# Optimization experiments

Measured on AMD Instinct MI355X. Metric: run time of the kernel, lower is better.

Reference implementation:

```python
import jax, jax.numpy as jnp
import numpy as np

N_USER = 50000
N_ITEM = 50000
D_IN = 128
D_OUT = 128
N_EDGE = 600000


def _sage(x_src, x_dst, ei, Wl, bl, Wr):
    # PyG SAGEConv: out = lin_l(mean_{j in N(i)} x_j) + lin_r(x_i)
    # lin_l has bias, lin_r has no bias. Weights are [out, in].
    src, dst = ei[0], ei[1]
    n_dst = x_dst.shape[0]
    msg = x_src[src]                                            # [E, D_in] gather
    agg = jax.ops.segment_sum(msg, dst, num_segments=n_dst)     # [N_dst, D_in]
    cnt = jax.ops.segment_sum(jnp.ones((ei.shape[1],), x_src.dtype), dst,
                              num_segments=n_dst)
    mean = agg / jnp.maximum(cnt, 1.0)[:, None]                 # isolated nodes -> 0
    return mean @ Wl.T + bl + x_dst @ Wr.T


def setup_inputs() -> dict:
    key = jax.random.key(0)
    ks = jax.random.split(key, 16)
    inp = {
        "x_user": jax.random.normal(ks[0], (N_USER, D_IN), jnp.float32),
        "x_item": jax.random.normal(ks[1], (N_ITEM, D_IN), jnp.float32),
        "ei_rates": jax.random.randint(ks[2], (2, N_EDGE), 0, N_USER, jnp.int64 if jax.config.jax_enable_x64 else jnp.int32),
        "ei_rev": jax.random.randint(ks[3], (2, N_EDGE), 0, N_USER, jnp.int64 if jax.config.jax_enable_x64 else jnp.int32),
        "ei_follows": jax.random.randint(ks[4], (2, N_EDGE), 0, N_USER, jnp.int64 if jax.config.jax_enable_x64 else jnp.int32),
    }
    s = 1.0 / np.sqrt(D_IN)
    names = ["rates", "rev", "fol"]
    for i, nm in enumerate(names):
        inp[f"Wl_{nm}"] = jax.random.uniform(ks[5 + 3 * i], (D_OUT, D_IN), jnp.float32, -s, s)
        inp[f"bl_{nm}"] = jax.random.uniform(ks[6 + 3 * i], (D_OUT,), jnp.float32, -s, s)
        inp[f"Wr_{nm}"] = jax.random.uniform(ks[7 + 3 * i], (D_OUT, D_IN), jnp.float32, -s, s)
    return inp


def reference(x_user, x_item, ei_rates, ei_rev, ei_follows,
              Wl_rates, bl_rates, Wr_rates,
              Wl_rev, bl_rev, Wr_rev,
              Wl_fol, bl_fol, Wr_fol):
    # relation (user -rates-> item): src=user, dst=item
    out_item = _sage(x_user, x_item, ei_rates, Wl_rates, bl_rates, Wr_rates)
    # relation (item -rev_rates-> user): src=item, dst=user
    out_user_rev = _sage(x_item, x_user, ei_rev, Wl_rev, bl_rev, Wr_rev)
    # relation (user -follows-> user)
    out_user_fol = _sage(x_user, x_user, ei_follows, Wl_fol, bl_fol, Wr_fol)
    # HeteroConv aggr='mean': average relation outputs per dst node type
    out_user = (out_user_rev + out_user_fol) * 0.5
    return out_user, out_item
```

## Files before the change

kernel.cpp:

```cpp
#include <hip/hip_runtime.h>

#define D 128
#define NBB 392

typedef __attribute__((ext_vector_type(8))) short bf16x8;
typedef __attribute__((ext_vector_type(4))) float f32x4;

__device__ inline unsigned short f2bf(float f) {
  unsigned u = __builtin_bit_cast(unsigned, f);
  unsigned r = u + 0x7FFFu + ((u >> 16) & 1u);
  return (unsigned short)(r >> 16);
}
__device__ inline float bf2f(unsigned short b) {
  unsigned u = ((unsigned)b) << 16;
  return __builtin_bit_cast(float, u);
}

struct SetupArgs {
  const float* xu; const float* xi;
  unsigned short* xbu; unsigned short* xbi;
  int n4u, n4i, nbConv;
  const int* ei[3]; int ne[3]; int nbh[3]; int nbHist;
  int* bh;
  const float* Wl_rates; const float* Wr_rates; const float* bl_rates;
  const float* Wl_rev;   const float* Wr_rev;   const float* bl_rev;
  const float* Wl_fol;   const float* Wr_fol;   const float* bl_fol;
  unsigned short* Wb_user; unsigned short* Wb_item;
  float* b_user; float* b_item;
};

__global__ void __launch_bounds__(256) setup_kernel(SetupArgs S) {
  const int tid = threadIdx.x;
  int b = blockIdx.x;
  if (b < S.nbConv) {
    int i = b * 256 + tid;
    const float* x;
    unsigned short* xb;
    if (i < S.n4u) { x = S.xu; xb = S.xbu; }
    else { i -= S.n4u; if (i >= S.n4i) return; x = S.xi; xb = S.xbi; }
    float4 v = ((const float4*)x)[i];
    ushort4 o;
    o.x = f2bf(v.x); o.y = f2bf(v.y); o.z = f2bf(v.z); o.w = f2bf(v.w);
    ((ushort4*)xb)[i] = o;
    return;
  }
  b -= S.nbConv;
  if (b < S.nbHist) {
    int rel = 0;
    while (b >= S.nbh[rel]) { b -= S.nbh[rel]; rel++; }
    __shared__ int lh[NBB];
    for (int t = tid; t < NBB; t += 256) lh[t] = 0;
    __syncthreads();
    const int ne = S.ne[rel];
    const int* dsts = S.ei[rel] + ne;
    const int base = b * 2048;
#pragma unroll
    for (int k = 0; k < 8; k++) {
      int i = base + k * 256 + tid;
      if (i < ne) atomicAdd(&lh[dsts[i] >> 7], 1);
    }
    __syncthreads();
    for (int t = tid; t < NBB; t += 256)
      if (lh[t]) atomicAdd(&S.bh[rel * NBB + t], lh[t]);
    return;
  }
  b -= S.nbHist;
  int idx = b * 256 + tid;
  if (idx >= 128 * 384) return;
  int n = idx / 384, k = idx - n * 384;
  float v;
  if (k < 128)      v = 0.5f * S.Wl_rev[n * 128 + k];
  else if (k < 256) v = 0.5f * S.Wl_fol[n * 128 + (k - 128)];
  else              v = 0.5f * (S.Wr_rev[n * 128 + (k - 256)] + S.Wr_fol[n * 128 + (k - 256)]);
  S.Wb_user[n * 384 + k] = f2bf(v);
  if (k < 256) {
    float w = (k < 128) ? S.Wl_rates[n * 128 + k] : S.Wr_rates[n * 128 + (k - 128)];
    S.Wb_item[n * 256 + k] = f2bf(w);
  }
  if (idx < 128) {
    S.b_item[idx] = S.bl_rates[idx];
    S.b_user[idx] = 0.5f * (S.bl_rev[idx] + S.bl_fol[idx]);
  }
}

__global__ void __launch_bounds__(192) scanb_kernel(const int* __restrict__ bh,
                                                    int* __restrict__ bbase,
                                                    int* __restrict__ bcur, int nbkt) {
  int w = threadIdx.x >> 6, l = threadIdx.x & 63;
  if (w >= 3) return;
  const int off = w * NBB;
  int v[7];
  int s0 = 0;
#pragma unroll
  for (int k = 0; k < 7; k++) {
    int idx = l * 7 + k;
    v[k] = (idx < nbkt) ? bh[off + idx] : 0;
    s0 += v[k];
  }
  int s = s0;
  for (int dlt = 1; dlt < 64; dlt <<= 1) {
    int t = __shfl_up(s, dlt);
    if (l >= dlt) s += t;
  }
  int run = s - s0;
#pragma unroll
  for (int k = 0; k < 7; k++) {
    int idx = l * 7 + k;
    if (idx < nbkt) { bbase[off + idx] = run; bcur[off + idx] = run; run += v[k]; }
  }
  if (l == 63) bbase[off + nbkt] = run;
}

struct PArgs { const int* ei[3]; int ne[3]; int nb[3]; unsigned* part[3]; };

__global__ void __launch_bounds__(256) part_kernel(PArgs P, int* __restrict__ bcur,
                                                   int nbkt) {
  int b = blockIdx.x, rel = 0;
  while (b >= P.nb[rel]) { b -= P.nb[rel]; rel++; }
  const int ne = P.ne[rel];
  const int* src = P.ei[rel];
  const int* dst = src + ne;
  const int base = b * 4096;
  const int tn = min(4096, ne - base);
  __shared__ int lh[NBB], lscan[NBB], gb[NBB], lcur[NBB];
  __shared__ uint2 pairs[4096];
  const int tid = threadIdx.x;
  for (int t = tid; t < NBB; t += 256) lh[t] = 0;
  __syncthreads();
#pragma unroll
  for (int k = 0; k < 16; k++) {
    int i = base + k * 256 + tid;
    if (i < ne) atomicAdd(&lh[dst[i] >> 7], 1);
  }
  __syncthreads();
  if (tid < 64) {
    int v[7];
    int s0 = 0;
#pragma unroll
    for (int k = 0; k < 7; k++) {
      int idx = tid * 7 + k;
      v[k] = (idx < NBB) ? lh[idx] : 0;
      s0 += v[k];
    }
    int s = s0;
    for (int dlt = 1; dlt < 64; dlt <<= 1) {
      int t = __shfl_up(s, dlt);
      if (tid >= dlt) s += t;
    }
    int run = s - s0;
#pragma unroll
    for (int k = 0; k < 7; k++) {
      int idx = tid * 7 + k;
      if (idx < NBB) { lscan[idx] = run; run += v[k]; }
    }
  }
  __syncthreads();
  for (int t = tid; t < nbkt; t += 256) {
    int c = lh[t];
    gb[t] = c ? atomicAdd(&bcur[rel * NBB + t], c) : 0;
    lcur[t] = lscan[t];
  }
  __syncthreads();
#pragma unroll
  for (int k = 0; k < 16; k++) {
    int i = base + k * 256 + tid;
    if (i < ne) {
      int d = dst[i];
      int slot = atomicAdd(&lcur[d >> 7], 1);
      pairs[slot] = (uint2){(unsigned)src[i], (unsigned)d};
    }
  }
  __syncthreads();
  unsigned* __restrict__ out = P.part[rel];
#pragma unroll
  for (int k = 0; k < 16; k++) {
    int slot = k * 256 + tid;
    if (slot < tn) {
      uint2 p = pairs[slot];
      int bin = (int)(p.y >> 7);
      out[gb[bin] + (slot - lscan[bin])] = p.x | ((p.y & 127u) << 25);
    }
  }
}

struct BAArgs {
  const unsigned* part[3];
  const unsigned short* xb[3];
  unsigned short* mean[3];
  int m[3];
};

__global__ void __launch_bounds__(512) bagg_kernel(BAArgs A, const int* __restrict__ bbase,
                                                   int nbkt) {
  const int rel = blockIdx.x / nbkt;
  const int b = blockIdx.x - rel * nbkt;
  const int bs = bbase[rel * NBB + b];
  const int be = bbase[rel * NBB + b + 1];
  const int n = be - bs;
  const unsigned* __restrict__ pp = A.part[rel] + bs;
  const unsigned short* __restrict__ x = A.xb[rel];
  unsigned short* __restrict__ mean = A.mean[rel];
  const int m = A.m[rel];
  const int tid = threadIdx.x;
  const int w = tid >> 6, lane = tid & 63;
  const size_t loff = (size_t)lane * 2;
  __shared__ unsigned sorted[4096];
  __shared__ int lcnt[128], lofs[128], lcur[128];

  if (n > 4096) {
    for (int r = w; r < 128; r += 8) {
      int gdst = b * 128 + r;
      if (gdst >= m) break;
      float a0 = 0.f, a1 = 0.f;
      int cnt = 0;
      for (int j = 0; j < n; j++) {
        unsigned p = pp[j];
        if ((int)(p >> 25) == r) {
          unsigned v = *(const unsigned*)(x + (size_t)(p & 0x1FFFFFFu) * D + loff);
          a0 += bf2f((unsigned short)(v & 0xFFFFu));
          a1 += bf2f((unsigned short)(v >> 16));
          cnt++;
        }
      }
      float inv = 1.0f / (float)max(cnt, 1);
      unsigned o = (unsigned)f2bf(a0 * inv) | ((unsigned)f2bf(a1 * inv) << 16);
      *(unsigned*)(mean + (size_t)gdst * D + loff) = o;
    }
    return;
  }

  if (tid < 128) lcnt[tid] = 0;
  __syncthreads();
  for (int i = tid; i < n; i += 512) atomicAdd(&lcnt[pp[i] >> 25], 1);
  __syncthreads();
  if (tid < 64) {
    int v0 = lcnt[2 * tid], v1 = lcnt[2 * tid + 1];
    int s0 = v0 + v1, s = s0;
    for (int dlt = 1; dlt < 64; dlt <<= 1) {
      int t = __shfl_up(s, dlt);
      if (tid >= dlt) s += t;
    }
    int ex = s - s0;
    lofs[2 * tid] = ex;
    lofs[2 * tid + 1] = ex + v0;
  }
  __syncthreads();
  if (tid < 128) lcur[tid] = lofs[tid];
  __syncthreads();
  for (int i = tid; i < n; i += 512) {
    unsigned p = pp[i];
    int slot = atomicAdd(&lcur[p >> 25], 1);
    sorted[slot] = p;
  }
  __syncthreads();

  const int r0 = w * 16, r1 = r0 + 16;
  int j = lofs[r0];
  const int jend = lcur[r1 - 1];
  int cur = r0;
  float a0 = 0.f, a1 = 0.f;

  auto putrow = [&](int r, float s0, float s1) {
    int g = b * 128 + r;
    if (g < m) {
      float inv = 1.0f / (float)max(lcur[r] - lofs[r], 1);
      unsigned o = (unsigned)f2bf(s0 * inv) | ((unsigned)f2bf(s1 * inv) << 16);
      *(unsigned*)(mean + (size_t)g * D + loff) = o;
    }
  };

#define STEP(pk, vk)                                                     \
  {                                                                      \
    int rk = (int)((pk) >> 25);                                          \
    if (rk != cur) {                                                     \
      putrow(cur, a0, a1);                                               \
      for (int z = cur + 1; z < rk; z++) putrow(z, 0.f, 0.f);            \
      cur = rk; a0 = 0.f; a1 = 0.f;                                      \
    }                                                                    \
    a0 += bf2f((unsigned short)((vk) & 0xFFFFu));                        \
    a1 += bf2f((unsigned short)((vk) >> 16));                            \
  }

  while (j + 8 <= jend) {
    unsigned p0 = sorted[j],     p1 = sorted[j + 1];
    unsigned p2 = sorted[j + 2], p3 = sorted[j + 3];
    unsigned p4 = sorted[j + 4], p5 = sorted[j + 5];
    unsigned p6 = sorted[j + 6], p7 = sorted[j + 7];
    unsigned v0 = *(const unsigned*)(x + (size_t)(p0 & 0x1FFFFFFu) * D + loff);
    unsigned v1 = *(const unsigned*)(x + (size_t)(p1 & 0x1FFFFFFu) * D + loff);
    unsigned v2 = *(const unsigned*)(x + (size_t)(p2 & 0x1FFFFFFu) * D + loff);
    unsigned v3 = *(const unsigned*)(x + (size_t)(p3 & 0x1FFFFFFu) * D + loff);
    unsigned v4 = *(const unsigned*)(x + (size_t)(p4 & 0x1FFFFFFu) * D + loff);
    unsigned v5 = *(const unsigned*)(x + (size_t)(p5 & 0x1FFFFFFu) * D + loff);
    unsigned v6 = *(const unsigned*)(x + (size_t)(p6 & 0x1FFFFFFu) * D + loff);
    unsigned v7 = *(const unsigned*)(x + (size_t)(p7 & 0x1FFFFFFu) * D + loff);
    STEP(p0, v0) STEP(p1, v1) STEP(p2, v2) STEP(p3, v3)
    STEP(p4, v4) STEP(p5, v5) STEP(p6, v6) STEP(p7, v7)
    j += 8;
  }
  for (; j < jend; j++) {
    unsigned p = sorted[j];
    unsigned v = *(const unsigned*)(x + (size_t)(p & 0x1FFFFFFu) * D + loff);
    STEP(p, v)
  }
#undef STEP
  putrow(cur, a0, a1);
  for (int z = cur + 1; z < r1; z++) putrow(z, 0.f, 0.f);
}

struct BSrcs { const unsigned short* s[3]; };
struct GemmArgs {
  BSrcs su, si;
  const unsigned short* wbU; const unsigned short* wbI;
  const float* bU; const float* bI;
  float* outU; float* outI;
  int MU, MI, nbU;
};

__global__ void __launch_bounds__(256) gemm2_kernel(GemmArgs A) {
  const bool isU = (int)blockIdx.x < A.nbU;
  const int bid = isU ? blockIdx.x : blockIdx.x - A.nbU;
  const BSrcs S = isU ? A.su : A.si;
  const unsigned short* __restrict__ Wb = isU ? A.wbU : A.wbI;
  const int K = isU ? 384 : 256;
  const float* __restrict__ bias = isU ? A.bU : A.bI;
  float* __restrict__ out = isU ? A.outU : A.outI;
  const int M = isU ? A.MU : A.MI;

  __shared__ __align__(16) unsigned short As[128][72];
  __shared__ __align__(16) unsigned short Ws[128][72];
  const int tid = threadIdx.x;
  const int lane = tid & 63;
  const int wave = tid >> 6;
  const int wr = (wave >> 1) * 64;
  const int wc = (wave & 1) * 64;
  const int l15 = lane & 15;
  const int quad = lane >> 4;
  const int m0 = bid * 128;

  f32x4 acc[4][4];
#pragma unroll
  for (int r = 0; r < 4; r++)
#pragma unroll
    for (int c = 0; c < 4; c++) acc[r][c] = (f32x4){0.f, 0.f, 0.f, 0.f};

  const int srow = tid >> 1, shalf = tid & 1;
  const int nchunks = K >> 6;
  for (int ch = 0; ch < nchunks; ch++) {
    const unsigned short* sp = S.s[ch >> 1];
    const int coff = (ch & 1) << 6;
    {
      int mm = min(m0 + srow, M - 1);
      const uint4* g = (const uint4*)(sp + (size_t)mm * D + coff + shalf * 32);
      uint4* ld = (uint4*)(&As[srow][shalf * 32]);
      ld[0] = g[0]; ld[1] = g[1]; ld[2] = g[2]; ld[3] = g[3];
    }
    {
      const uint4* g = (const uint4*)(Wb + (size_t)srow * K + ch * 64 + shalf * 32);
      uint4* ld = (uint4*)(&Ws[srow][shalf * 32]);
      ld[0] = g[0]; ld[1] = g[1]; ld[2] = g[2]; ld[3] = g[3];
    }
    __syncthreads();
#pragma unroll
    for (int kk = 0; kk < 64; kk += 32) {
      const int kb = kk + quad * 8;
      bf16x8 a0 = *(const bf16x8*)&As[wr + l15][kb];
      bf16x8 a1 = *(const bf16x8*)&As[wr + 16 + l15][kb];
      bf16x8 a2 = *(const bf16x8*)&As[wr + 32 + l15][kb];
      bf16x8 a3 = *(const bf16x8*)&As[wr + 48 + l15][kb];
      bf16x8 b0 = *(const bf16x8*)&Ws[wc + l15][kb];
      bf16x8 b1 = *(const bf16x8*)&Ws[wc + 16 + l15][kb];
      bf16x8 b2 = *(const bf16x8*)&Ws[wc + 32 + l15][kb];
      bf16x8 b3 = *(const bf16x8*)&Ws[wc + 48 + l15][kb];
      acc[0][0] = __builtin_amdgcn_mfma_f32_16x16x32_bf16(a0, b0, acc[0][0], 0, 0, 0);
      acc[0][1] = __builtin_amdgcn_mfma_f32_16x16x32_bf16(a0, b1, acc[0][1], 0, 0, 0);
      acc[0][2] = __builtin_amdgcn_mfma_f32_16x16x32_bf16(a0, b2, acc[0][2], 0, 0, 0);
      acc[0][3] = __builtin_amdgcn_mfma_f32_16x16x32_bf16(a0, b3, acc[0][3], 0, 0, 0);
      acc[1][0] = __builtin_amdgcn_mfma_f32_16x16x32_bf16(a1, b0, acc[1][0], 0, 0, 0);
      acc[1][1] = __builtin_amdgcn_mfma_f32_16x16x32_bf16(a1, b1, acc[1][1], 0, 0, 0);
      acc[1][2] = __builtin_amdgcn_mfma_f32_16x16x32_bf16(a1, b2, acc[1][2], 0, 0, 0);
      acc[1][3] = __builtin_amdgcn_mfma_f32_16x16x32_bf16(a1, b3, acc[1][3], 0, 0, 0);
      acc[2][0] = __builtin_amdgcn_mfma_f32_16x16x32_bf16(a2, b0, acc[2][0], 0, 0, 0);
      acc[2][1] = __builtin_amdgcn_mfma_f32_16x16x32_bf16(a2, b1, acc[2][1], 0, 0, 0);
      acc[2][2] = __builtin_amdgcn_mfma_f32_16x16x32_bf16(a2, b2, acc[2][2], 0, 0, 0);
      acc[2][3] = __builtin_amdgcn_mfma_f32_16x16x32_bf16(a2, b3, acc[2][3], 0, 0, 0);
      acc[3][0] = __builtin_amdgcn_mfma_f32_16x16x32_bf16(a3, b0, acc[3][0], 0, 0, 0);
      acc[3][1] = __builtin_amdgcn_mfma_f32_16x16x32_bf16(a3, b1, acc[3][1], 0, 0, 0);
      acc[3][2] = __builtin_amdgcn_mfma_f32_16x16x32_bf16(a3, b2, acc[3][2], 0, 0, 0);
      acc[3][3] = __builtin_amdgcn_mfma_f32_16x16x32_bf16(a3, b3, acc[3][3], 0, 0, 0);
    }
    __syncthreads();
  }
#pragma unroll
  for (int c = 0; c < 4; c++) {
    const int n = wc + c * 16 + l15;
    const float bv = bias[n];
#pragma unroll
    for (int r = 0; r < 4; r++) {
      const int mrow = m0 + wr + r * 16 + quad * 4;
#pragma unroll
      for (int i = 0; i < 4; i++) {
        if (mrow + i < M) out[(size_t)(mrow + i) * D + n] = acc[r][c][i] + bv;
      }
    }
  }
}

extern "C" void kernel_launch(void* const* d_in, const int* in_sizes, int n_in,
                              void* d_out, int out_size, void* d_ws, size_t ws_size,
                              hipStream_t stream) {
  const float* x_user   = (const float*)d_in[0];
  const float* x_item   = (const float*)d_in[1];
  const int*   ei_rates = (const int*)d_in[2];
  const int*   ei_rev   = (const int*)d_in[3];
  const int*   ei_fol   = (const int*)d_in[4];
  const float* Wl_rates = (const float*)d_in[5];
  const float* bl_rates = (const float*)d_in[6];
  const float* Wr_rates = (const float*)d_in[7];
  const float* Wl_rev   = (const float*)d_in[8];
  const float* bl_rev   = (const float*)d_in[9];
  const float* Wr_rev   = (const float*)d_in[10];
  const float* Wl_fol   = (const float*)d_in[11];
  const float* bl_fol   = (const float*)d_in[12];
  const float* Wr_fol   = (const float*)d_in[13];

  const int NU = in_sizes[0] / D;
  const int NI = in_sizes[1] / D;
  const int E_rates = in_sizes[2] / 2;
  const int E_rev   = in_sizes[3] / 2;
  const int E_fol   = in_sizes[4] / 2;
  const int nbkt = ((NU > NI ? NU : NI) + 127) / 128;

  char* wsb = (char*)d_ws;
  size_t off = 0;
  auto take = [&](size_t bytes) {
    char* p = wsb + off;
    off += (bytes + 15) & ~(size_t)15;
    return p;
  };
  int* bhist = (int*)take(3 * NBB * 4);
  const size_t zero_bytes = off;
  int* bbase = (int*)take(3 * NBB * 4);
  int* bcur  = (int*)take(3 * NBB * 4);
  unsigned* part_rates = (unsigned*)take((size_t)E_rates * 4);
  unsigned* part_rev   = (unsigned*)take((size_t)E_rev * 4);
  unsigned* part_fol   = (unsigned*)take((size_t)E_fol * 4);
  unsigned short* xb_user    = (unsigned short*)take((size_t)NU * D * 2);
  unsigned short* xb_item    = (unsigned short*)take((size_t)NI * D * 2);
  unsigned short* mean_rates = (unsigned short*)take((size_t)NI * D * 2);
  unsigned short* mean_rev   = (unsigned short*)take((size_t)NU * D * 2);
  unsigned short* mean_fol   = (unsigned short*)take((size_t)NU * D * 2);
  unsigned short* Wb_user    = (unsigned short*)take(128 * 384 * 2);
  unsigned short* Wb_item    = (unsigned short*)take(128 * 256 * 2);
  float* b_user = (float*)take(128 * 4);
  float* b_item = (float*)take(128 * 4);

  hipMemsetAsync(d_ws, 0, zero_bytes, stream);

  SetupArgs SA;
  SA.xu = x_user; SA.xi = x_item; SA.xbu = xb_user; SA.xbi = xb_item;
  SA.n4u = NU * D / 4; SA.n4i = NI * D / 4;
  SA.nbConv = (SA.n4u + SA.n4i + 255) / 256;
  SA.ei[0] = ei_rates; SA.ne[0] = E_rates; SA.nbh[0] = (E_rates + 2047) / 2048;
  SA.ei[1] = ei_rev;   SA.ne[1] = E_rev;   SA.nbh[1] = (E_rev + 2047) / 2048;
  SA.ei[2] = ei_fol;   SA.ne[2] = E_fol;   SA.nbh[2] = (E_fol + 2047) / 2048;
  SA.nbHist = SA.nbh[0] + SA.nbh[1] + SA.nbh[2];
  SA.bh = bhist;
  SA.Wl_rates = Wl_rates; SA.Wr_rates = Wr_rates; SA.bl_rates = bl_rates;
  SA.Wl_rev = Wl_rev; SA.Wr_rev = Wr_rev; SA.bl_rev = bl_rev;
  SA.Wl_fol = Wl_fol; SA.Wr_fol = Wr_fol; SA.bl_fol = bl_fol;
  SA.Wb_user = Wb_user; SA.Wb_item = Wb_item;
  SA.b_user = b_user; SA.b_item = b_item;
  const int nbPrep = (128 * 384 + 255) / 256;
  setup_kernel<<<SA.nbConv + SA.nbHist + nbPrep, 256, 0, stream>>>(SA);

  scanb_kernel<<<1, 192, 0, stream>>>(bhist, bbase, bcur, nbkt);

  PArgs P;
  P.ei[0] = ei_rates; P.ne[0] = E_rates; P.nb[0] = (E_rates + 4095) / 4096; P.part[0] = part_rates;
  P.ei[1] = ei_rev;   P.ne[1] = E_rev;   P.nb[1] = (E_rev + 4095) / 4096;   P.part[1] = part_rev;
  P.ei[2] = ei_fol;   P.ne[2] = E_fol;   P.nb[2] = (E_fol + 4095) / 4096;   P.part[2] = part_fol;
  part_kernel<<<P.nb[0] + P.nb[1] + P.nb[2], 256, 0, stream>>>(P, bcur, nbkt);

  BAArgs BA;
  BA.part[0] = part_rates; BA.xb[0] = xb_user; BA.mean[0] = mean_rates; BA.m[0] = NI;
  BA.part[1] = part_rev;   BA.xb[1] = xb_item; BA.mean[1] = mean_rev;   BA.m[1] = NU;
  BA.part[2] = part_fol;   BA.xb[2] = xb_user; BA.mean[2] = mean_fol;   BA.m[2] = NU;
  bagg_kernel<<<3 * nbkt, 512, 0, stream>>>(BA, bbase, nbkt);

  GemmArgs gma;
  gma.su.s[0] = mean_rev;   gma.su.s[1] = mean_fol; gma.su.s[2] = xb_user;
  gma.si.s[0] = mean_rates; gma.si.s[1] = xb_item;  gma.si.s[2] = nullptr;
  gma.wbU = Wb_user; gma.wbI = Wb_item;
  gma.bU = b_user;   gma.bI = b_item;
  gma.outU = (float*)d_out;
  gma.outI = (float*)d_out + (size_t)NU * D;
  gma.MU = NU; gma.MI = NI;
  gma.nbU = (NU + 127) / 128;
  const int nbI = (NI + 127) / 128;
  gemm2_kernel<<<gma.nbU + nbI, 256, 0, stream>>>(gma);
}
```

Measured before the change: 314.1 us.

## Split bucket aggregation into separate sort and fine-grained gather kernels

The fused bucket-aggregate kernel is replaced by two kernels. A sort kernel orders each bucket's edges by destination row into global memory and records CSR row starts. A gather kernel then uses many smaller blocks, each covering 64 rows, to do the mean aggregation. This drops the 16KB shared-memory buffer and the slow fallback path for buckets over 4096 edges, and raises occupancy and the number of blocks for the gather. The cost is an extra launch and a global round-trip of the sorted edge arrays.

```diff
diff --git a/kernel.cpp b/kernel.cpp
--- a/kernel.cpp
+++ b/kernel.cpp
@@ -183,55 +183,29 @@
   }
 }
 
-struct BAArgs {
+struct SortArgs {
   const unsigned* part[3];
-  const unsigned short* xb[3];
-  unsigned short* mean[3];
-  int m[3];
+  unsigned* sg[3];
+  int* rowstart;
+  int Rp1;
 };
 
-__global__ void __launch_bounds__(512) bagg_kernel(BAArgs A, const int* __restrict__ bbase,
+__global__ void __launch_bounds__(256) sort_kernel(SortArgs S, const int* __restrict__ bbase,
                                                    int nbkt) {
   const int rel = blockIdx.x / nbkt;
   const int b = blockIdx.x - rel * nbkt;
   const int bs = bbase[rel * NBB + b];
   const int be = bbase[rel * NBB + b + 1];
   const int n = be - bs;
-  const unsigned* __restrict__ pp = A.part[rel] + bs;
-  const unsigned short* __restrict__ x = A.xb[rel];
-  unsigned short* __restrict__ mean = A.mean[rel];
-  const int m = A.m[rel];
+  const unsigned* __restrict__ pp = S.part[rel] + bs;
+  unsigned* __restrict__ out = S.sg[rel] + bs;
+  int* __restrict__ rs = S.rowstart + rel * S.Rp1;
   const int tid = threadIdx.x;
-  const int w = tid >> 6, lane = tid & 63;
-  const size_t loff = (size_t)lane * 2;
-  __shared__ unsigned sorted[4096];
   __shared__ int lcnt[128], lofs[128], lcur[128];
 
-  if (n > 4096) {
-    for (int r = w; r < 128; r += 8) {
-      int gdst = b * 128 + r;
-      if (gdst >= m) break;
-      float a0 = 0.f, a1 = 0.f;
-      int cnt = 0;
-      for (int j = 0; j < n; j++) {
-        unsigned p = pp[j];
-        if ((int)(p >> 25) == r) {
-          unsigned v = *(const unsigned*)(x + (size_t)(p & 0x1FFFFFFu) * D + loff);
-          a0 += bf2f((unsigned short)(v & 0xFFFFu));
-          a1 += bf2f((unsigned short)(v >> 16));
-          cnt++;
-        }
-      }
-      float inv = 1.0f / (float)max(cnt, 1);
-      unsigned o = (unsigned)f2bf(a0 * inv) | ((unsigned)f2bf(a1 * inv) << 16);
-      *(unsigned*)(mean + (size_t)gdst * D + loff) = o;
-    }
-    return;
-  }
-
   if (tid < 128) lcnt[tid] = 0;
   __syncthreads();
-  for (int i = tid; i < n; i += 512) atomicAdd(&lcnt[pp[i] >> 25], 1);
+  for (int i = tid; i < n; i += 256) atomicAdd(&lcnt[pp[i] >> 25], 1);
   __syncthreads();
   if (tid < 64) {
     int v0 = lcnt[2 * tid], v1 = lcnt[2 * tid + 1];
@@ -245,25 +219,51 @@
     lofs[2 * tid + 1] = ex + v0;
   }
   __syncthreads();
-  if (tid < 128) lcur[tid] = lofs[tid];
-  __syncthreads();
-  for (int i = tid; i < n; i += 512) {
+  if (tid < 128) {
+    lcur[tid] = lofs[tid];
+    rs[b * 128 + tid] = bs + lofs[tid];
+  }
+  if (tid == 128 && b == nbkt - 1) rs[nbkt * 128] = be;
+  __syncthreads();
+  for (int i = tid; i < n; i += 256) {
     unsigned p = pp[i];
     int slot = atomicAdd(&lcur[p >> 25], 1);
-    sorted[slot] = p;
-  }
-  __syncthreads();
-
-  const int r0 = w * 16, r1 = r0 + 16;
-  int j = lofs[r0];
-  const int jend = lcur[r1 - 1];
-  int cur = r0;
+    out[slot] = p;
+  }
+}
+
+struct GArgs {
+  const unsigned* sg[3];
+  const unsigned short* xb[3];
+  unsigned short* mean[3];
+  int m[3];
+};
+
+__global__ void __launch_bounds__(256) gather_kernel(GArgs A, const int* __restrict__ rowstart,
+                                                     int nbpr, int Rp1) {
+  const int rel = blockIdx.x / nbpr;
+  const int blk = blockIdx.x - rel * nbpr;
+  const unsigned* __restrict__ sg = A.sg[rel];
+  const unsigned short* __restrict__ x = A.xb[rel];
+  unsigned short* __restrict__ mean = A.mean[rel];
+  const int m = A.m[rel];
+  const int* __restrict__ rs = rowstart + rel * Rp1;
+  const int tid = threadIdx.x;
+  const int w = tid >> 6, lane = tid & 63;
+  const size_t loff = (size_t)lane * 2;
+
+  const int gbase = blk * 64 + w * 16;
+  const int f0 = gbase & 127;
+  const int bkt = gbase - f0;
+  int j = rs[gbase];
+  const int jend = rs[gbase + 16];
+  int cur = f0;
   float a0 = 0.f, a1 = 0.f;
 
-  auto putrow = [&](int r, float s0, float s1) {
-    int g = b * 128 + r;
+  auto putrow = [&](int rf, float s0, float s1) {
+    int g = bkt + rf;
     if (g < m) {
-      float inv = 1.0f / (float)max(lcur[r] - lofs[r], 1);
+      float inv = 1.0f / (float)max(rs[g + 1] - rs[g], 1);
       unsigned o = (unsigned)f2bf(s0 * inv) | ((unsigned)f2bf(s1 * inv) << 16);
       *(unsigned*)(mean + (size_t)g * D + loff) = o;
     }
@@ -282,10 +282,10 @@
   }
 
   while (j + 8 <= jend) {
-    unsigned p0 = sorted[j],     p1 = sorted[j + 1];
-    unsigned p2 = sorted[j + 2], p3 = sorted[j + 3];
-    unsigned p4 = sorted[j + 4], p5 = sorted[j + 5];
-    unsigned p6 = sorted[j + 6], p7 = sorted[j + 7];
+    unsigned p0 = sg[j],     p1 = sg[j + 1];
+    unsigned p2 = sg[j + 2], p3 = sg[j + 3];
+    unsigned p4 = sg[j + 4], p5 = sg[j + 5];
+    unsigned p6 = sg[j + 6], p7 = sg[j + 7];
     unsigned v0 = *(const unsigned*)(x + (size_t)(p0 & 0x1FFFFFFu) * D + loff);
     unsigned v1 = *(const unsigned*)(x + (size_t)(p1 & 0x1FFFFFFu) * D + loff);
     unsigned v2 = *(const unsigned*)(x + (size_t)(p2 & 0x1FFFFFFu) * D + loff);
@@ -299,13 +299,13 @@
     j += 8;
   }
   for (; j < jend; j++) {
-    unsigned p = sorted[j];
+    unsigned p = sg[j];
     unsigned v = *(const unsigned*)(x + (size_t)(p & 0x1FFFFFFu) * D + loff);
     STEP(p, v)
   }
 #undef STEP
   putrow(cur, a0, a1);
-  for (int z = cur + 1; z < r1; z++) putrow(z, 0.f, 0.f);
+  for (int z = cur + 1; z < f0 + 16; z++) putrow(z, 0.f, 0.f);
 }
 
 struct BSrcs { const unsigned short* s[3]; };
@@ -430,6 +430,9 @@
   const int E_rev   = in_sizes[3] / 2;
   const int E_fol   = in_sizes[4] / 2;
   const int nbkt = ((NU > NI ? NU : NI) + 127) / 128;
+  const int Rtot = nbkt * 128;
+  const int Rp1 = Rtot + 1;
+  const int nbpr = Rtot / 64;
 
   char* wsb = (char*)d_ws;
   size_t off = 0;
@@ -445,6 +448,10 @@
   unsigned* part_rates = (unsigned*)take((size_t)E_rates * 4);
   unsigned* part_rev   = (unsigned*)take((size_t)E_rev * 4);
   unsigned* part_fol   = (unsigned*)take((size_t)E_fol * 4);
+  unsigned* sg_rates   = (unsigned*)take((size_t)E_rates * 4);
+  unsigned* sg_rev     = (unsigned*)take((size_t)E_rev * 4);
+  unsigned* sg_fol     = (unsigned*)take((size_t)E_fol * 4);
+  int* rowstart        = (int*)take((size_t)3 * Rp1 * 4);
   unsigned short* xb_user    = (unsigned short*)take((size_t)NU * D * 2);
   unsigned short* xb_item    = (unsigned short*)take((size_t)NI * D * 2);
   unsigned short* mean_rates = (unsigned short*)take((size_t)NI * D * 2);
@@ -482,11 +489,18 @@
   P.ei[2] = ei_fol;   P.ne[2] = E_fol;   P.nb[2] = (E_fol + 4095) / 4096;   P.part[2] = part_fol;
   part_kernel<<<P.nb[0] + P.nb[1] + P.nb[2], 256, 0, stream>>>(P, bcur, nbkt);
 
-  BAArgs BA;
-  BA.part[0] = part_rates; BA.xb[0] = xb_user; BA.mean[0] = mean_rates; BA.m[0] = NI;
-  BA.part[1] = part_rev;   BA.xb[1] = xb_item; BA.mean[1] = mean_rev;   BA.m[1] = NU;
-  BA.part[2] = part_fol;   BA.xb[2] = xb_user; BA.mean[2] = mean_fol;   BA.m[2] = NU;
-  bagg_kernel<<<3 * nbkt, 512, 0, stream>>>(BA, bbase, nbkt);
+  SortArgs SS;
+  SS.part[0] = part_rates; SS.sg[0] = sg_rates;
+  SS.part[1] = part_rev;   SS.sg[1] = sg_rev;
+  SS.part[2] = part_fol;   SS.sg[2] = sg_fol;
+  SS.rowstart = rowstart; SS.Rp1 = Rp1;
+  sort_kernel<<<3 * nbkt, 256, 0, stream>>>(SS, bbase, nbkt);
+
+  GArgs GA;
+  GA.sg[0] = sg_rates; GA.xb[0] = xb_user; GA.mean[0] = mean_rates; GA.m[0] = NI;
+  GA.sg[1] = sg_rev;   GA.xb[1] = xb_item; GA.mean[1] = mean_rev;   GA.m[1] = NU;
+  GA.sg[2] = sg_fol;   GA.xb[2] = xb_user; GA.mean[2] = mean_fol;   GA.m[2] = NU;
+  gather_kernel<<<3 * nbpr, 256, 0, stream>>>(GA, rowstart, nbpr, Rp1);
 
   GemmArgs gma;
   gma.su.s[0] = mean_rev;   gma.su.s[1] = mean_fol; gma.su.s[2] = xb_user;
```

Result: slower. 334.6 us (+6.5%).
